# Kernel tuning notes

Hardware: AMD Instinct MI355X
Metric: run time of the kernel (lower is better)

## Reference

```python
import jax, jax.numpy as jnp
import numpy as np

NEG_SLOPE = 0.2
EPS = 1e-16


def _gat_layer(x, src, dst, W, a_src, a_dst, b, n_nodes):
    # x: [N, Fin], W: [Fout, Fin]; src/dst: [E'] (self-loops already appended)
    h = x @ W.T                              # [N, Fout]
    alpha_s = h @ a_src                      # [N] per-source score
    alpha_d = h @ a_dst                      # [N] per-dest score
    e = jax.nn.leaky_relu(alpha_s[src] + alpha_d[dst], NEG_SLOPE)  # [E']
    # segment softmax over destination nodes (PyG softmax semantics)
    m = jax.ops.segment_max(e, dst, num_segments=n_nodes)          # [N]
    ex = jnp.exp(e - m[dst])                                       # [E']
    s = jax.ops.segment_sum(ex, dst, num_segments=n_nodes)         # [N]
    alpha = ex / (s[dst] + EPS)                                    # [E']
    out = jax.ops.segment_sum(alpha[:, None] * h[src], dst, num_segments=n_nodes)
    return out + b, alpha


def setup_inputs() -> dict:
    key = jax.random.key(0)
    ks = jax.random.split(key, 14)
    N, E, F_IN, H1, H2, F_OUT = 50000, 800000, 128, 64, 64, 32
    sc = 0.1
    return {
        "x": jax.random.normal(ks[0], (N, F_IN), dtype=jnp.float32),
        "edge_index": jax.random.randint(ks[1], (2, E), 0, N, dtype=jnp.int64),
        "W1": jax.random.normal(ks[2], (H1, F_IN), dtype=jnp.float32) * sc,
        "a_src1": jax.random.normal(ks[3], (H1,), dtype=jnp.float32) * sc,
        "a_dst1": jax.random.normal(ks[4], (H1,), dtype=jnp.float32) * sc,
        "b1": jnp.zeros((H1,), dtype=jnp.float32),
        "W2": jax.random.normal(ks[5], (H2, H1), dtype=jnp.float32) * sc,
        "a_src2": jax.random.normal(ks[6], (H2,), dtype=jnp.float32) * sc,
        "a_dst2": jax.random.normal(ks[7], (H2,), dtype=jnp.float32) * sc,
        "b2": jnp.zeros((H2,), dtype=jnp.float32),
        "W3": jax.random.normal(ks[8], (F_OUT, H2), dtype=jnp.float32) * sc,
        "a_src3": jax.random.normal(ks[9], (F_OUT,), dtype=jnp.float32) * sc,
        "a_dst3": jax.random.normal(ks[10], (F_OUT,), dtype=jnp.float32) * sc,
        "b3": jnp.zeros((F_OUT,), dtype=jnp.float32),
    }


def reference(x, edge_index, W1, a_src1, a_dst1, b1, W2, a_src2, a_dst2, b2, W3, a_src3, a_dst3, b3):
    N = x.shape[0]
    loops = jnp.arange(N, dtype=edge_index.dtype)
    src = jnp.concatenate([edge_index[0], loops])  # add_self_loops=True
    dst = jnp.concatenate([edge_index[1], loops])

    h, alpha1 = _gat_layer(x, src, dst, W1, a_src1, a_dst1, b1, N)
    h = jax.nn.relu(h)
    h, _ = _gat_layer(h, src, dst, W2, a_src2, a_dst2, b2, N)
    h = jax.nn.relu(h)
    out, _ = _gat_layer(h, src, dst, W3, a_src3, a_dst3, b3, N)
    # att_tuple = (edge_index with self loops, attention coefficients of layer 1)
    return (jnp.stack([src, dst]), alpha1, out)
```

## Files before the change

kernel.cpp:

```cpp
#include <hip/hip_runtime.h>
#include <hip/hip_bf16.h>
#include <math.h>

#define NEG_SLOPE 0.2f
#define GAT_EPS 1e-16f

constexpr int NN = 50000;
constexpr int NE = 800000;
constexpr int EP = NE + NN;
constexpr int NB = (NN + 255) / 256;

constexpr int PB  = 128;
constexpr int PT  = 1024;
constexpr int CH  = (EP + PB - 1) / PB;
constexpr int NCH = 4;
constexpr int BPC = PB / NCH;

__device__ inline void edge_sd(const int* __restrict__ ei, int i, int& s, int& d) {
    if (i < NE) { s = ei[i]; d = ei[NE + i]; }
    else        { s = d = i - NE; }
}

__device__ inline float bflo(unsigned int h) { return __uint_as_float(h << 16); }
__device__ inline float bfhi(unsigned int h) { return __uint_as_float(h & 0xffff0000u); }

__global__ __launch_bounds__(PT) void k_p1_hist(const int* __restrict__ ei,
                                                float* __restrict__ out0,
                                                unsigned char* __restrict__ hist,
                                                unsigned char* __restrict__ rank8) {
    __shared__ unsigned int sh[NN / 4];
    int b = blockIdx.x, t = threadIdx.x;
    for (int w = t; w < NN / 4; w += PT) sh[w] = 0u;
    __syncthreads();
    int i0 = b * CH;
    int iend = i0 + CH; if (iend > EP) iend = EP;
    for (int i = i0 + t; i < iend; i += PT) {
        int s, d; edge_sd(ei, i, s, d);
        __builtin_nontemporal_store((float)s, &out0[i]);
        __builtin_nontemporal_store((float)d, &out0[EP + i]);
        int sft = (d & 3) * 8;
        unsigned int old = atomicAdd(&sh[d >> 2], 1u << sft);
        __builtin_nontemporal_store((unsigned char)(old >> sft), &rank8[i]);
    }
    __syncthreads();
    unsigned int* hw = (unsigned int*)(hist + (size_t)b * NN);
    for (int w = t; w < NN / 4; w += PT) hw[w] = sh[w];
}

__global__ __launch_bounds__(256) void k_p2s1(unsigned char* __restrict__ hist,
                                              unsigned char* __restrict__ chunkoff,
                                              int* __restrict__ rowptr,
                                              int* __restrict__ bsum) {
    __shared__ int sh[256];
    int t = threadIdx.x;
    int n = blockIdx.x * 256 + t;
    int v = 0;
    if (n < NN) {
        unsigned int runs[NCH];
#pragma unroll
        for (int c = 0; c < NCH; ++c) {
            size_t base = (size_t)(c * BPC) * NN + n;
            unsigned int vv[BPC];
#pragma unroll
            for (int b = 0; b < BPC; ++b) vv[b] = hist[base + (size_t)b * NN];
            unsigned int run = 0;
#pragma unroll
            for (int b = 0; b < BPC; ++b) { unsigned int x = vv[b]; vv[b] = run; run += x; }
#pragma unroll
            for (int b = 0; b < BPC; ++b) hist[base + (size_t)b * NN] = (unsigned char)vv[b];
            runs[c] = run;
        }
        unsigned int o1 = runs[0], o2 = o1 + runs[1], o3 = o2 + runs[2];
        *(unsigned int*)&chunkoff[(size_t)n * 4] = (o1 << 8) | (o2 << 16) | (o3 << 24);
        v = (int)(o3 + runs[3]);
    }
    sh[t] = v; __syncthreads();
    for (int off = 1; off < 256; off <<= 1) {
        int x = (t >= off) ? sh[t - off] : 0;
        __syncthreads();
        sh[t] += x;
        __syncthreads();
    }
    if (n < NN) rowptr[n] = sh[t] - v;
    if (t == 255) bsum[blockIdx.x] = sh[255];
}

__global__ __launch_bounds__(256) void k_s23(int* __restrict__ rowptr,
                                             const int* __restrict__ bsum) {
    __shared__ int sh[256];
    int t = threadIdx.x;
    int v = (t < NB) ? bsum[t] : 0;
    sh[t] = v; __syncthreads();
    for (int off = 1; off < 256; off <<= 1) {
        int x = (t >= off) ? sh[t - off] : 0;
        __syncthreads();
        sh[t] += x;
        __syncthreads();
    }
    int blk = blockIdx.x;
    int off = (blk == 0) ? 0 : sh[blk - 1];
    int n = blk * 256 + t;
    if (n < NN) rowptr[n] += off;
    if (n == 0) rowptr[NN] = EP;
}

__global__ __launch_bounds__(256) void k_fill(const int* __restrict__ ei,
                                              const unsigned char* __restrict__ rank8,
                                              const unsigned char* __restrict__ hist,
                                              const unsigned char* __restrict__ chunkoff,
                                              const int* __restrict__ rowptr,
                                              unsigned short* __restrict__ col) {
    int i = blockIdx.x * 256 + threadIdx.x;
    if (i >= EP) return;
    int b = i / CH;
    int c = b / BPC;
    int s, d; edge_sd(ei, i, s, d);
    int pos = rowptr[d] + (int)chunkoff[d * 4 + c] + (int)hist[(size_t)b * NN + d]
            + (int)rank8[i];
    col[pos] = (unsigned short)s;
}

__global__ void k_alpha_out(const int* __restrict__ ei, const float* __restrict__ as_,
                            const float* __restrict__ ad_, const float* __restrict__ inv,
                            float* __restrict__ out_alpha) {
    int i = blockIdx.x * blockDim.x + threadIdx.x;
    if (i >= EP) return;
    int s, d; edge_sd(ei, i, s, d);
    float v = as_[s] + ad_[d];
    v = v > 0.f ? v : NEG_SLOPE * v;
    __builtin_nontemporal_store(__expf(v) * inv[d], &out_alpha[i]);
}

struct alignas(8) bh4 { __hip_bfloat16 a, b, c, d; };

__device__ inline void fma4(float4& acc, float x, const float4& w) {
    acc.x = fmaf(x, w.x, acc.x);
    acc.y = fmaf(x, w.y, acc.y);
    acc.z = fmaf(x, w.z, acc.z);
    acc.w = fmaf(x, w.w, acc.w);
}

template <int FIN, int FOUT, int NPB>
__global__ __launch_bounds__(256) void k_gemm_t(const float* __restrict__ in,
                                                const float* __restrict__ W,
                                                const float* __restrict__ avs,
                                                const float* __restrict__ avd,
                                                __hip_bfloat16* __restrict__ H,
                                                float* __restrict__ as_,
                                                float* __restrict__ ad_, int n) {
    constexpr int TF = FOUT / 4;
    constexpr int XS = FIN + 4;
    constexpr int WS = FOUT + 4;
    __shared__ float sX[NPB * XS];
    __shared__ float sWt[FIN * WS];
    int tid = threadIdx.x;
    for (int idx = tid; idx < FIN * FOUT; idx += 256) {
        int f = idx % FOUT, k = idx / FOUT;
        sWt[k * WS + f] = W[f * FIN + k];
    }
    int nb = blockIdx.x * NPB;
    for (int idx = tid; idx < NPB * (FIN / 4); idx += 256) {
        int node = idx / (FIN / 4), kq = idx % (FIN / 4);
        int g = nb + node;
        float4 v = make_float4(0.f, 0.f, 0.f, 0.f);
        if (g < n) v = *(const float4*)&in[(size_t)g * FIN + kq * 4];
        *(float4*)&sX[node * XS + kq * 4] = v;
    }
    __syncthreads();

    int fq = tid % TF, ng = tid / TF;
    int n0 = ng * 4;
    float4 acc0 = make_float4(0.f, 0.f, 0.f, 0.f);
    float4 acc1 = acc0, acc2 = acc0, acc3 = acc0;
    for (int k = 0; k < FIN; k += 4) {
        float4 w0 = *(const float4*)&sWt[(k + 0) * WS + fq * 4];
        float4 w1 = *(const float4*)&sWt[(k + 1) * WS + fq * 4];
        float4 w2 = *(const float4*)&sWt[(k + 2) * WS + fq * 4];
        float4 w3 = *(const float4*)&sWt[(k + 3) * WS + fq * 4];
        float4 x0 = *(const float4*)&sX[(n0 + 0) * XS + k];
        float4 x1 = *(const float4*)&sX[(n0 + 1) * XS + k];
        float4 x2 = *(const float4*)&sX[(n0 + 2) * XS + k];
        float4 x3 = *(const float4*)&sX[(n0 + 3) * XS + k];
        fma4(acc0, x0.x, w0); fma4(acc0, x0.y, w1); fma4(acc0, x0.z, w2); fma4(acc0, x0.w, w3);
        fma4(acc1, x1.x, w0); fma4(acc1, x1.y, w1); fma4(acc1, x1.z, w2); fma4(acc1, x1.w, w3);
        fma4(acc2, x2.x, w0); fma4(acc2, x2.y, w1); fma4(acc2, x2.z, w2); fma4(acc2, x2.w, w3);
        fma4(acc3, x3.x, w0); fma4(acc3, x3.y, w1); fma4(acc3, x3.z, w2); fma4(acc3, x3.w, w3);
    }
    float4 accs[4] = {acc0, acc1, acc2, acc3};
    float4 vs4 = *(const float4*)&avs[fq * 4];
    float4 vd4 = *(const float4*)&avd[fq * 4];
#pragma unroll
    for (int j = 0; j < 4; ++j) {
        int g = nb + n0 + j;
        float ps = accs[j].x * vs4.x + accs[j].y * vs4.y + accs[j].z * vs4.z + accs[j].w * vs4.w;
        float pd = accs[j].x * vd4.x + accs[j].y * vd4.y + accs[j].z * vd4.z + accs[j].w * vd4.w;
#pragma unroll
        for (int off = TF / 2; off; off >>= 1) {
            ps += __shfl_down(ps, off, TF);
            pd += __shfl_down(pd, off, TF);
        }
        if (g < n) {
            if (fq == 0) { as_[g] = ps; ad_[g] = pd; }
            bh4 o;
            o.a = __float2bfloat16(accs[j].x);
            o.b = __float2bfloat16(accs[j].y);
            o.c = __float2bfloat16(accs[j].z);
            o.d = __float2bfloat16(accs[j].w);
            *(bh4*)&H[(size_t)g * FOUT + fq * 4] = o;
        }
    }
}

template <int FOUT, bool RELU, bool WRITE_INV>
__global__ __launch_bounds__(256) void k_node_attn(
    const int* __restrict__ rowptr, const unsigned short* __restrict__ col,
    const float* __restrict__ as_, const float* __restrict__ ad_,
    const __hip_bfloat16* __restrict__ H, const float* __restrict__ bias,
    float* __restrict__ outp, float* __restrict__ inv_out) {
    int wid = (blockIdx.x * blockDim.x + threadIdx.x) >> 6;
    int lane = threadIdx.x & 63;
    if (wid >= NN) return;
    int start = rowptr[wid], end = rowptr[wid + 1];
    float adv = ad_[wid];
    const uint2* __restrict__ H4 = (const uint2*)H;

    float sloc = 0.f;
    float ax = 0.f, ay = 0.f, az = 0.f, aw = 0.f;
    for (int c = start; c < end; c += 64) {
        int e = c + lane;
        float p = 0.f;
        int sc = 0;
        if (e < end) {
            sc = (int)col[e];
            float v = as_[sc] + adv;
            v = v > 0.f ? v : NEG_SLOPE * v;
            p = __expf(v);
        }
        sloc += p;
        int cnt = end - c; if (cnt > 64) cnt = 64;
        if (FOUT == 64) {
            int q = lane >> 4, fl = lane & 15;
            int j = 0;
            for (; j + 32 <= cnt; j += 32) {
                float pp[8]; int ss[8]; uint2 hh[8];
#pragma unroll
                for (int k = 0; k < 8; ++k) {
                    int ek = j + 4 * k + q;
                    pp[k] = __shfl(p, ek);
                    ss[k] = __shfl(sc, ek);
                }
#pragma unroll
                for (int k = 0; k < 8; ++k) hh[k] = H4[((size_t)ss[k] << 4) + fl];
#pragma unroll
                for (int k = 0; k < 8; ++k) {
                    ax = fmaf(pp[k], bflo(hh[k].x), ax);
                    ay = fmaf(pp[k], bfhi(hh[k].x), ay);
                    az = fmaf(pp[k], bflo(hh[k].y), az);
                    aw = fmaf(pp[k], bfhi(hh[k].y), aw);
                }
            }
            for (; j + 8 <= cnt; j += 8) {
                int e0 = j + q, e1 = j + 4 + q;
                float p0 = __shfl(p, e0), p1 = __shfl(p, e1);
                int s0 = __shfl(sc, e0), s1 = __shfl(sc, e1);
                uint2 h0 = H4[((size_t)s0 << 4) + fl];
                uint2 h1 = H4[((size_t)s1 << 4) + fl];
                ax = fmaf(p0, bflo(h0.x), ax); ay = fmaf(p0, bfhi(h0.x), ay);
                az = fmaf(p0, bflo(h0.y), az); aw = fmaf(p0, bfhi(h0.y), aw);
                ax = fmaf(p1, bflo(h1.x), ax); ay = fmaf(p1, bfhi(h1.x), ay);
                az = fmaf(p1, bflo(h1.y), az); aw = fmaf(p1, bfhi(h1.y), aw);
            }
            for (; j < cnt; j += 4) {
                int e0 = j + q;
                float p0 = __shfl(p, e0);
                int   s0 = __shfl(sc, e0);
                uint2 h0 = H4[((size_t)s0 << 4) + fl];
                ax = fmaf(p0, bflo(h0.x), ax); ay = fmaf(p0, bfhi(h0.x), ay);
                az = fmaf(p0, bflo(h0.y), az); aw = fmaf(p0, bfhi(h0.y), aw);
            }
        } else {
            int oc = lane >> 3, fl = lane & 7;
            int j = 0;
            for (; j + 32 <= cnt; j += 32) {
                float pp[4]; int ss[4]; uint2 hh[4];
#pragma unroll
                for (int k = 0; k < 4; ++k) {
                    int ek = j + 8 * k + oc;
                    pp[k] = __shfl(p, ek);
                    ss[k] = __shfl(sc, ek);
                }
#pragma unroll
                for (int k = 0; k < 4; ++k) hh[k] = H4[((size_t)ss[k] << 3) + fl];
#pragma unroll
                for (int k = 0; k < 4; ++k) {
                    ax = fmaf(pp[k], bflo(hh[k].x), ax);
                    ay = fmaf(pp[k], bfhi(hh[k].x), ay);
                    az = fmaf(pp[k], bflo(hh[k].y), az);
                    aw = fmaf(pp[k], bfhi(hh[k].y), aw);
                }
            }
            for (; j < cnt; j += 8) {
                int e0 = j + oc;
                float p0 = __shfl(p, e0);
                int   s0 = __shfl(sc, e0);
                uint2 h0 = H4[((size_t)s0 << 3) + fl];
                ax = fmaf(p0, bflo(h0.x), ax); ay = fmaf(p0, bfhi(h0.x), ay);
                az = fmaf(p0, bflo(h0.y), az); aw = fmaf(p0, bfhi(h0.y), aw);
            }
        }
    }
    for (int off = 32; off; off >>= 1) sloc += __shfl_xor(sloc, off);
    float inv = 1.f / (sloc + GAT_EPS);
    if (WRITE_INV && lane == 0) inv_out[wid] = inv;

    if (FOUT == 64) {
        ax += __shfl_xor(ax, 16); ay += __shfl_xor(ay, 16);
        az += __shfl_xor(az, 16); aw += __shfl_xor(aw, 16);
        ax += __shfl_xor(ax, 32); ay += __shfl_xor(ay, 32);
        az += __shfl_xor(az, 32); aw += __shfl_xor(aw, 32);
        if (lane < 16) {
            float4 bb = *(const float4*)&bias[lane * 4];
            float o0 = bb.x + ax * inv;
            float o1 = bb.y + ay * inv;
            float o2 = bb.z + az * inv;
            float o3 = bb.w + aw * inv;
            if (RELU) {
                o0 = fmaxf(o0, 0.f); o1 = fmaxf(o1, 0.f);
                o2 = fmaxf(o2, 0.f); o3 = fmaxf(o3, 0.f);
            }
            *(float4*)&outp[((size_t)wid << 6) + lane * 4] = make_float4(o0, o1, o2, o3);
        }
    } else {
        ax += __shfl_xor(ax, 8);  ay += __shfl_xor(ay, 8);
        az += __shfl_xor(az, 8);  aw += __shfl_xor(aw, 8);
        ax += __shfl_xor(ax, 16); ay += __shfl_xor(ay, 16);
        az += __shfl_xor(az, 16); aw += __shfl_xor(aw, 16);
        ax += __shfl_xor(ax, 32); ay += __shfl_xor(ay, 32);
        az += __shfl_xor(az, 32); aw += __shfl_xor(aw, 32);
        if (lane < 8) {
            float4 bb = *(const float4*)&bias[lane * 4];
            float o0 = bb.x + ax * inv;
            float o1 = bb.y + ay * inv;
            float o2 = bb.z + az * inv;
            float o3 = bb.w + aw * inv;
            if (RELU) {
                o0 = fmaxf(o0, 0.f); o1 = fmaxf(o1, 0.f);
                o2 = fmaxf(o2, 0.f); o3 = fmaxf(o3, 0.f);
            }
            *(float4*)&outp[((size_t)wid << 5) + lane * 4] = make_float4(o0, o1, o2, o3);
        }
    }
}

extern "C" void kernel_launch(void* const* d_in, const int* in_sizes, int n_in,
                              void* d_out, int out_size, void* d_ws, size_t ws_size,
                              hipStream_t stream) {
    const float* x  = (const float*)d_in[0];
    const int*   ei = (const int*)d_in[1];
    const float* W1 = (const float*)d_in[2];
    const float* as1 = (const float*)d_in[3];
    const float* ad1 = (const float*)d_in[4];
    const float* b1 = (const float*)d_in[5];
    const float* W2 = (const float*)d_in[6];
    const float* as2 = (const float*)d_in[7];
    const float* ad2 = (const float*)d_in[8];
    const float* b2 = (const float*)d_in[9];
    const float* W3 = (const float*)d_in[10];
    const float* as3 = (const float*)d_in[11];
    const float* ad3 = (const float*)d_in[12];
    const float* b3 = (const float*)d_in[13];

    float* out = (float*)d_out;
    float* out_edges = out;
    float* out_alpha = out + 2 * EP;
    float* out_final = out + 3 * EP;

    char* w = (char*)d_ws;
    size_t o = 0;
    auto alloc = [&](size_t bytes) { void* p = w + o; o = (o + bytes + 15) & ~15ull; return p; };
    float* as_ = (float*)alloc((size_t)NN * 4);
    float* ad_ = (float*)alloc((size_t)NN * 4);
    float* inv = (float*)alloc((size_t)NN * 4);
    __hip_bfloat16* H = (__hip_bfloat16*)alloc((size_t)NN * 64 * 2);
    int* rowptr = (int*)alloc((size_t)(NN + 1) * 4);
    unsigned char* rank8 = (unsigned char*)alloc((size_t)EP);
    unsigned short* col  = (unsigned short*)alloc((size_t)EP * 2);
    unsigned char* chunkoff = (unsigned char*)alloc((size_t)NN * 4);
    int* bsum = (int*)alloc(1024);

    const size_t aggBytes  = (size_t)NN * 64 * 4;
    const size_t histBytes = (size_t)PB * NN;
    float* agg = (ws_size >= o + aggBytes)
        ? (float*)(w + o)
        : (float*)d_in[0];
    unsigned char* hist = (ws_size >= o + aggBytes + histBytes)
        ? (unsigned char*)(w + o + aggBytes)
        : (unsigned char*)out_final;

    k_p1_hist<<<PB, PT, 0, stream>>>(ei, out_edges, hist, rank8);
    k_p2s1<<<NB, 256, 0, stream>>>(hist, chunkoff, rowptr, bsum);
    k_s23<<<NB, 256, 0, stream>>>(rowptr, bsum);
    k_fill<<<(EP + 255) / 256, 256, 0, stream>>>(ei, rank8, hist, chunkoff, rowptr, col);

    const int nblk = (NN * 64 + 255) / 256;

    k_gemm_t<128, 64, 64><<<(NN + 63) / 64, 256, 0, stream>>>(x, W1, as1, ad1, H, as_, ad_, NN);
    k_node_attn<64, true, true><<<nblk, 256, 0, stream>>>(rowptr, col, as_, ad_, H, b1,
                                                          agg, inv);
    k_alpha_out<<<(EP + 255) / 256, 256, 0, stream>>>(ei, as_, ad_, inv, out_alpha);

    k_gemm_t<64, 64, 64><<<(NN + 63) / 64, 256, 0, stream>>>(agg, W2, as2, ad2, H, as_, ad_, NN);
    k_node_attn<64, true, false><<<nblk, 256, 0, stream>>>(rowptr, col, as_, ad_, H, b2,
                                                           agg, nullptr);

    k_gemm_t<64, 32, 128><<<(NN + 127) / 128, 256, 0, stream>>>(agg, W3, as3, ad3, H, as_, ad_,
                                                                NN);
    k_node_attn<32, false, false><<<nblk, 256, 0, stream>>>(rowptr, col, as_, ad_, H, b3,
                                                            out_final, nullptr);
}
```

Before: 292.7 us.

## Fuse attention aggregation with next layer's linear transform and scores

Adds a kernel that aggregates attention-weighted neighbor features per destination node, applies bias and ReLU, then multiplies by the next layer's weight matrix held in shared memory and computes the next layer's source/destination scores. This removes two separate GEMM launches and the fp32 intermediate round trip through global memory. Separate H/score buffers per layer avoid read-write hazards. It also drops the 8-edge unrolled tail in the old aggregation kernel. The risk is that each block now stages the weights in shared memory and each wave does extra shuffle work, which could lower occupancy.

```diff
diff --git a/kernel.cpp b/kernel.cpp
--- a/kernel.cpp
+++ b/kernel.cpp
@@ -211,6 +211,150 @@
     }
 }
 
+template <int GOUT, bool WRITE_INV>
+__global__ __launch_bounds__(256) void k_attn_gemm(
+    const int* __restrict__ rowptr, const unsigned short* __restrict__ col,
+    const float* __restrict__ as_, const float* __restrict__ ad_,
+    const __hip_bfloat16* __restrict__ H, const float* __restrict__ bias,
+    const float* __restrict__ Wn,
+    const float* __restrict__ avs, const float* __restrict__ avd,
+    __hip_bfloat16* __restrict__ Hout,
+    float* __restrict__ as_out, float* __restrict__ ad_out,
+    float* __restrict__ inv_out) {
+    __shared__ float sW[64 * GOUT];
+    int tid = threadIdx.x;
+    for (int idx = tid; idx < 64 * GOUT; idx += 256) {
+        int f = idx % GOUT, k = idx / GOUT;
+        sW[k * GOUT + f] = Wn[f * 64 + k];
+    }
+    __syncthreads();
+
+    int wid = (blockIdx.x * blockDim.x + tid) >> 6;
+    int lane = tid & 63;
+    if (wid >= NN) return;
+    int start = rowptr[wid], end = rowptr[wid + 1];
+    float adv = ad_[wid];
+    const uint2* __restrict__ H4 = (const uint2*)H;
+
+    float sloc = 0.f;
+    float ax = 0.f, ay = 0.f, az = 0.f, aw = 0.f;
+    for (int c = start; c < end; c += 64) {
+        int e = c + lane;
+        float p = 0.f;
+        int sc = 0;
+        if (e < end) {
+            sc = (int)col[e];
+            float v = as_[sc] + adv;
+            v = v > 0.f ? v : NEG_SLOPE * v;
+            p = __expf(v);
+        }
+        sloc += p;
+        int cnt = end - c; if (cnt > 64) cnt = 64;
+        int q = lane >> 4, fl = lane & 15;
+        int j = 0;
+        for (; j + 32 <= cnt; j += 32) {
+            float pp[8]; int ss[8]; uint2 hh[8];
+#pragma unroll
+            for (int k = 0; k < 8; ++k) {
+                int ek = j + 4 * k + q;
+                pp[k] = __shfl(p, ek);
+                ss[k] = __shfl(sc, ek);
+            }
+#pragma unroll
+            for (int k = 0; k < 8; ++k) hh[k] = H4[((size_t)ss[k] << 4) + fl];
+#pragma unroll
+            for (int k = 0; k < 8; ++k) {
+                ax = fmaf(pp[k], bflo(hh[k].x), ax);
+                ay = fmaf(pp[k], bfhi(hh[k].x), ay);
+                az = fmaf(pp[k], bflo(hh[k].y), az);
+                aw = fmaf(pp[k], bfhi(hh[k].y), aw);
+            }
+        }
+        for (; j + 8 <= cnt; j += 8) {
+            int e0 = j + q, e1 = j + 4 + q;
+            float p0 = __shfl(p, e0), p1 = __shfl(p, e1);
+            int s0 = __shfl(sc, e0), s1 = __shfl(sc, e1);
+            uint2 h0 = H4[((size_t)s0 << 4) + fl];
+            uint2 h1 = H4[((size_t)s1 << 4) + fl];
+            ax = fmaf(p0, bflo(h0.x), ax); ay = fmaf(p0, bfhi(h0.x), ay);
+            az = fmaf(p0, bflo(h0.y), az); aw = fmaf(p0, bfhi(h0.y), aw);
+            ax = fmaf(p1, bflo(h1.x), ax); ay = fmaf(p1, bfhi(h1.x), ay);
+            az = fmaf(p1, bflo(h1.y), az); aw = fmaf(p1, bfhi(h1.y), aw);
+        }
+        for (; j < cnt; j += 4) {
+            int e0 = j + q;
+            float p0 = __shfl(p, e0);
+            int   s0 = __shfl(sc, e0);
+            uint2 h0 = H4[((size_t)s0 << 4) + fl];
+            ax = fmaf(p0, bflo(h0.x), ax); ay = fmaf(p0, bfhi(h0.x), ay);
+            az = fmaf(p0, bflo(h0.y), az); aw = fmaf(p0, bfhi(h0.y), aw);
+        }
+    }
+    for (int off = 32; off; off >>= 1) sloc += __shfl_xor(sloc, off);
+    float inv = 1.f / (sloc + GAT_EPS);
+    if (WRITE_INV && lane == 0) inv_out[wid] = inv;
+
+    ax += __shfl_xor(ax, 16); ay += __shfl_xor(ay, 16);
+    az += __shfl_xor(az, 16); aw += __shfl_xor(aw, 16);
+    ax += __shfl_xor(ax, 32); ay += __shfl_xor(ay, 32);
+    az += __shfl_xor(az, 32); aw += __shfl_xor(aw, 32);
+
+    int fl = lane & 15;
+    float4 bb = *(const float4*)&bias[fl * 4];
+    float h0 = fmaxf(bb.x + ax * inv, 0.f);
+    float h1 = fmaxf(bb.y + ay * inv, 0.f);
+    float h2 = fmaxf(bb.z + az * inv, 0.f);
+    float h3 = fmaxf(bb.w + aw * inv, 0.f);
+
+    float acc = 0.f;
+    if (GOUT == 64) {
+        int f = lane;
+#pragma unroll
+        for (int m = 0; m < 16; ++m) {
+            float q0 = __shfl(h0, m), q1 = __shfl(h1, m);
+            float q2 = __shfl(h2, m), q3 = __shfl(h3, m);
+            acc = fmaf(q0, sW[(4 * m + 0) * 64 + f], acc);
+            acc = fmaf(q1, sW[(4 * m + 1) * 64 + f], acc);
+            acc = fmaf(q2, sW[(4 * m + 2) * 64 + f], acc);
+            acc = fmaf(q3, sW[(4 * m + 3) * 64 + f], acc);
+        }
+    } else {
+        int f = lane & 31, kh = lane >> 5;
+#pragma unroll
+        for (int mm = 0; mm < 8; ++mm) {
+            int m = 8 * kh + mm;
+            float q0 = __shfl(h0, m), q1 = __shfl(h1, m);
+            float q2 = __shfl(h2, m), q3 = __shfl(h3, m);
+            acc = fmaf(q0, sW[(4 * m + 0) * 32 + f], acc);
+            acc = fmaf(q1, sW[(4 * m + 1) * 32 + f], acc);
+            acc = fmaf(q2, sW[(4 * m + 2) * 32 + f], acc);
+            acc = fmaf(q3, sW[(4 * m + 3) * 32 + f], acc);
+        }
+        acc += __shfl_xor(acc, 32);
+    }
+
+    float ps, pd;
+    if (GOUT == 64) {
+        ps = acc * avs[lane];
+        pd = acc * avd[lane];
+    } else {
+        ps = (lane < 32) ? acc * avs[lane] : 0.f;
+        pd = (lane < 32) ? acc * avd[lane] : 0.f;
+    }
+#pragma unroll
+    for (int off = 32; off; off >>= 1) {
+        ps += __shfl_xor(ps, off);
+        pd += __shfl_xor(pd, off);
+    }
+    if (lane == 0) { as_out[wid] = ps; ad_out[wid] = pd; }
+
+    if (GOUT == 64) {
+        Hout[(size_t)wid * 64 + lane] = __float2bfloat16(acc);
+    } else if (lane < 32) {
+        Hout[(size_t)wid * 32 + lane] = __float2bfloat16(acc);
+    }
+}
+
 template <int FOUT, bool RELU, bool WRITE_INV>
 __global__ __launch_bounds__(256) void k_node_attn(
     const int* __restrict__ rowptr, const unsigned short* __restrict__ col,
@@ -258,17 +402,6 @@
                     az = fmaf(pp[k], bflo(hh[k].y), az);
                     aw = fmaf(pp[k], bfhi(hh[k].y), aw);
                 }
-            }
-            for (; j + 8 <= cnt; j += 8) {
-                int e0 = j + q, e1 = j + 4 + q;
-                float p0 = __shfl(p, e0), p1 = __shfl(p, e1);
-                int s0 = __shfl(sc, e0), s1 = __shfl(sc, e1);
-                uint2 h0 = H4[((size_t)s0 << 4) + fl];
-                uint2 h1 = H4[((size_t)s1 << 4) + fl];
-                ax = fmaf(p0, bflo(h0.x), ax); ay = fmaf(p0, bfhi(h0.x), ay);
-                az = fmaf(p0, bflo(h0.y), az); aw = fmaf(p0, bfhi(h0.y), aw);
-                ax = fmaf(p1, bflo(h1.x), ax); ay = fmaf(p1, bfhi(h1.x), ay);
-                az = fmaf(p1, bflo(h1.y), az); aw = fmaf(p1, bfhi(h1.y), aw);
             }
             for (; j < cnt; j += 4) {
                 int e0 = j + q;
@@ -378,23 +511,25 @@
     char* w = (char*)d_ws;
     size_t o = 0;
     auto alloc = [&](size_t bytes) { void* p = w + o; o = (o + bytes + 15) & ~15ull; return p; };
-    float* as_ = (float*)alloc((size_t)NN * 4);
-    float* ad_ = (float*)alloc((size_t)NN * 4);
+    float* asA = (float*)alloc((size_t)NN * 4);
+    float* adA = (float*)alloc((size_t)NN * 4);
+    float* asB = (float*)alloc((size_t)NN * 4);
+    float* adB = (float*)alloc((size_t)NN * 4);
+    float* asC = (float*)alloc((size_t)NN * 4);
+    float* adC = (float*)alloc((size_t)NN * 4);
     float* inv = (float*)alloc((size_t)NN * 4);
-    __hip_bfloat16* H = (__hip_bfloat16*)alloc((size_t)NN * 64 * 2);
+    __hip_bfloat16* H1 = (__hip_bfloat16*)alloc((size_t)NN * 64 * 2);
+    __hip_bfloat16* H2 = (__hip_bfloat16*)alloc((size_t)NN * 64 * 2);
+    __hip_bfloat16* H3 = (__hip_bfloat16*)alloc((size_t)NN * 32 * 2);
     int* rowptr = (int*)alloc((size_t)(NN + 1) * 4);
     unsigned char* rank8 = (unsigned char*)alloc((size_t)EP);
     unsigned short* col  = (unsigned short*)alloc((size_t)EP * 2);
     unsigned char* chunkoff = (unsigned char*)alloc((size_t)NN * 4);
     int* bsum = (int*)alloc(1024);
 
-    const size_t aggBytes  = (size_t)NN * 64 * 4;
     const size_t histBytes = (size_t)PB * NN;
-    float* agg = (ws_size >= o + aggBytes)
-        ? (float*)(w + o)
-        : (float*)d_in[0];
-    unsigned char* hist = (ws_size >= o + aggBytes + histBytes)
-        ? (unsigned char*)(w + o + aggBytes)
+    unsigned char* hist = (ws_size >= o + histBytes)
+        ? (unsigned char*)(w + o)
         : (unsigned char*)out_final;
 
     k_p1_hist<<<PB, PT, 0, stream>>>(ei, out_edges, hist, rank8);
@@ -404,17 +539,14 @@
 
     const int nblk = (NN * 64 + 255) / 256;
 
-    k_gemm_t<128, 64, 64><<<(NN + 63) / 64, 256, 0, stream>>>(x, W1, as1, ad1, H, as_, ad_, NN);
-    k_node_attn<64, true, true><<<nblk, 256, 0, stream>>>(rowptr, col, as_, ad_, H, b1,
-                                                          agg, inv);
-    k_alpha_out<<<(EP + 255) / 256, 256, 0, stream>>>(ei, as_, ad_, inv, out_alpha);
-
-    k_gemm_t<64, 64, 64><<<(NN + 63) / 64, 256, 0, stream>>>(agg, W2, as2, ad2, H, as_, ad_, NN);
-    k_node_attn<64, true, false><<<nblk, 256, 0, stream>>>(rowptr, col, as_, ad_, H, b2,
-                                                           agg, nullptr);
-
-    k_gemm_t<64, 32, 128><<<(NN + 127) / 128, 256, 0, stream>>>(agg, W3, as3, ad3, H, as_, ad_,
-                                                                NN);
-    k_node_attn<32, false, false><<<nblk, 256, 0, stream>>>(rowptr, col, as_, ad_, H, b3,
+    k_gemm_t<128, 64, 64><<<(NN + 63) / 64, 256, 0, stream>>>(x, W1, as1, ad1, H1,
+                                                              asA, adA, NN);
+    k_attn_gemm<64, true><<<nblk, 256, 0, stream>>>(rowptr, col, asA, adA, H1, b1,
+                                                    W2, as2, ad2, H2, asB, adB, inv);
+    k_alpha_out<<<(EP + 255) / 256, 256, 0, stream>>>(ei, asA, adA, inv, out_alpha);
+
+    k_attn_gemm<32, false><<<nblk, 256, 0, stream>>>(rowptr, col, asB, adB, H2, b2,
+                                                     W3, as3, ad3, H3, asC, adC, nullptr);
+    k_node_attn<32, false, false><<<nblk, 256, 0, stream>>>(rowptr, col, asC, adC, H3, b3,
                                                             out_final, nullptr);
 }
```

After: 390.1 us. 33.3% more time.

## Map multiple destination nodes per wavefront in attention aggregation

Applied to the files above, without the earlier changes.

The attention aggregation kernel now assigns a 16-lane (FOUT=64) or 8-lane (FOUT=32) group to each destination node instead of a full 64-lane wavefront, so one wave handles 4 or 8 nodes at once. Average degree is about 17, so a full wave per node left most lanes idle in the score phase and needed wide cross-lane reductions. Edges are processed 8 at a time per group, and per-group shuffles broadcast scores and source indices. The cost is fewer independent gathers in flight per node and load imbalance between nodes of different degree in the same wave.

```diff
diff --git a/kernel.cpp b/kernel.cpp
--- a/kernel.cpp
+++ b/kernel.cpp
@@ -212,144 +212,74 @@
 }
 
 template <int FOUT, bool RELU, bool WRITE_INV>
-__global__ __launch_bounds__(256) void k_node_attn(
+__global__ __launch_bounds__(256) void k_attn_grp(
     const int* __restrict__ rowptr, const unsigned short* __restrict__ col,
     const float* __restrict__ as_, const float* __restrict__ ad_,
     const __hip_bfloat16* __restrict__ H, const float* __restrict__ bias,
     float* __restrict__ outp, float* __restrict__ inv_out) {
-    int wid = (blockIdx.x * blockDim.x + threadIdx.x) >> 6;
+    constexpr int L = (FOUT == 64) ? 16 : 8;
+    constexpr int GPW = 64 / L;
+    int tid = blockIdx.x * 256 + threadIdx.x;
+    int wid = tid >> 6;
     int lane = threadIdx.x & 63;
-    if (wid >= NN) return;
-    int start = rowptr[wid], end = rowptr[wid + 1];
-    float adv = ad_[wid];
+    int grp = lane / L;
+    int gl  = lane & (L - 1);
+    int node = wid * GPW + grp;
+    if (node >= NN) return;
+
+    int start = rowptr[node], end = rowptr[node + 1];
+    float adv = ad_[node];
     const uint2* __restrict__ H4 = (const uint2*)H;
+    int base = lane & ~(L - 1);
 
     float sloc = 0.f;
-    float ax = 0.f, ay = 0.f, az = 0.f, aw = 0.f;
-    for (int c = start; c < end; c += 64) {
-        int e = c + lane;
+    float4 acc = make_float4(0.f, 0.f, 0.f, 0.f);
+    for (int c = start; c < end; c += 8) {
+        int e = c + gl;
         float p = 0.f;
         int sc = 0;
-        if (e < end) {
+        if (gl < 8 && e < end) {
             sc = (int)col[e];
             float v = as_[sc] + adv;
             v = v > 0.f ? v : NEG_SLOPE * v;
             p = __expf(v);
         }
         sloc += p;
-        int cnt = end - c; if (cnt > 64) cnt = 64;
-        if (FOUT == 64) {
-            int q = lane >> 4, fl = lane & 15;
-            int j = 0;
-            for (; j + 32 <= cnt; j += 32) {
-                float pp[8]; int ss[8]; uint2 hh[8];
-#pragma unroll
-                for (int k = 0; k < 8; ++k) {
-                    int ek = j + 4 * k + q;
-                    pp[k] = __shfl(p, ek);
-                    ss[k] = __shfl(sc, ek);
-                }
-#pragma unroll
-                for (int k = 0; k < 8; ++k) hh[k] = H4[((size_t)ss[k] << 4) + fl];
-#pragma unroll
-                for (int k = 0; k < 8; ++k) {
-                    ax = fmaf(pp[k], bflo(hh[k].x), ax);
-                    ay = fmaf(pp[k], bfhi(hh[k].x), ay);
-                    az = fmaf(pp[k], bflo(hh[k].y), az);
-                    aw = fmaf(pp[k], bfhi(hh[k].y), aw);
-                }
-            }
-            for (; j + 8 <= cnt; j += 8) {
-                int e0 = j + q, e1 = j + 4 + q;
-                float p0 = __shfl(p, e0), p1 = __shfl(p, e1);
-                int s0 = __shfl(sc, e0), s1 = __shfl(sc, e1);
-                uint2 h0 = H4[((size_t)s0 << 4) + fl];
-                uint2 h1 = H4[((size_t)s1 << 4) + fl];
-                ax = fmaf(p0, bflo(h0.x), ax); ay = fmaf(p0, bfhi(h0.x), ay);
-                az = fmaf(p0, bflo(h0.y), az); aw = fmaf(p0, bfhi(h0.y), aw);
-                ax = fmaf(p1, bflo(h1.x), ax); ay = fmaf(p1, bfhi(h1.x), ay);
-                az = fmaf(p1, bflo(h1.y), az); aw = fmaf(p1, bfhi(h1.y), aw);
-            }
-            for (; j < cnt; j += 4) {
-                int e0 = j + q;
-                float p0 = __shfl(p, e0);
-                int   s0 = __shfl(sc, e0);
-                uint2 h0 = H4[((size_t)s0 << 4) + fl];
-                ax = fmaf(p0, bflo(h0.x), ax); ay = fmaf(p0, bfhi(h0.x), ay);
-                az = fmaf(p0, bflo(h0.y), az); aw = fmaf(p0, bfhi(h0.y), aw);
-            }
-        } else {
-            int oc = lane >> 3, fl = lane & 7;
-            int j = 0;
-            for (; j + 32 <= cnt; j += 32) {
-                float pp[4]; int ss[4]; uint2 hh[4];
-#pragma unroll
-                for (int k = 0; k < 4; ++k) {
-                    int ek = j + 8 * k + oc;
-                    pp[k] = __shfl(p, ek);
-                    ss[k] = __shfl(sc, ek);
-                }
-#pragma unroll
-                for (int k = 0; k < 4; ++k) hh[k] = H4[((size_t)ss[k] << 3) + fl];
-#pragma unroll
-                for (int k = 0; k < 4; ++k) {
-                    ax = fmaf(pp[k], bflo(hh[k].x), ax);
-                    ay = fmaf(pp[k], bfhi(hh[k].x), ay);
-                    az = fmaf(pp[k], bflo(hh[k].y), az);
-                    aw = fmaf(pp[k], bfhi(hh[k].y), aw);
-                }
-            }
-            for (; j < cnt; j += 8) {
-                int e0 = j + oc;
-                float p0 = __shfl(p, e0);
-                int   s0 = __shfl(sc, e0);
-                uint2 h0 = H4[((size_t)s0 << 3) + fl];
-                ax = fmaf(p0, bflo(h0.x), ax); ay = fmaf(p0, bfhi(h0.x), ay);
-                az = fmaf(p0, bflo(h0.y), az); aw = fmaf(p0, bfhi(h0.y), aw);
-            }
-        }
-    }
-    for (int off = 32; off; off >>= 1) sloc += __shfl_xor(sloc, off);
+        int cnt = end - c; if (cnt > 8) cnt = 8;
+        float pp[8]; int ss[8]; uint2 hh[8];
+#pragma unroll
+        for (int k = 0; k < 8; ++k) {
+            pp[k] = __shfl(p, base + k);
+            ss[k] = __shfl(sc, base + k);
+        }
+#pragma unroll
+        for (int k = 0; k < 8; ++k) {
+            hh[k] = make_uint2(0u, 0u);
+            if (k < cnt) hh[k] = H4[(size_t)ss[k] * L + gl];
+        }
+#pragma unroll
+        for (int k = 0; k < 8; ++k) {
+            acc.x = fmaf(pp[k], bflo(hh[k].x), acc.x);
+            acc.y = fmaf(pp[k], bfhi(hh[k].x), acc.y);
+            acc.z = fmaf(pp[k], bflo(hh[k].y), acc.z);
+            acc.w = fmaf(pp[k], bfhi(hh[k].y), acc.w);
+        }
+    }
+#pragma unroll
+    for (int off = L / 2; off; off >>= 1) sloc += __shfl_xor(sloc, off);
     float inv = 1.f / (sloc + GAT_EPS);
-    if (WRITE_INV && lane == 0) inv_out[wid] = inv;
-
-    if (FOUT == 64) {
-        ax += __shfl_xor(ax, 16); ay += __shfl_xor(ay, 16);
-        az += __shfl_xor(az, 16); aw += __shfl_xor(aw, 16);
-        ax += __shfl_xor(ax, 32); ay += __shfl_xor(ay, 32);
-        az += __shfl_xor(az, 32); aw += __shfl_xor(aw, 32);
-        if (lane < 16) {
-            float4 bb = *(const float4*)&bias[lane * 4];
-            float o0 = bb.x + ax * inv;
-            float o1 = bb.y + ay * inv;
-            float o2 = bb.z + az * inv;
-            float o3 = bb.w + aw * inv;
-            if (RELU) {
-                o0 = fmaxf(o0, 0.f); o1 = fmaxf(o1, 0.f);
-                o2 = fmaxf(o2, 0.f); o3 = fmaxf(o3, 0.f);
-            }
-            *(float4*)&outp[((size_t)wid << 6) + lane * 4] = make_float4(o0, o1, o2, o3);
-        }
-    } else {
-        ax += __shfl_xor(ax, 8);  ay += __shfl_xor(ay, 8);
-        az += __shfl_xor(az, 8);  aw += __shfl_xor(aw, 8);
-        ax += __shfl_xor(ax, 16); ay += __shfl_xor(ay, 16);
-        az += __shfl_xor(az, 16); aw += __shfl_xor(aw, 16);
-        ax += __shfl_xor(ax, 32); ay += __shfl_xor(ay, 32);
-        az += __shfl_xor(az, 32); aw += __shfl_xor(aw, 32);
-        if (lane < 8) {
-            float4 bb = *(const float4*)&bias[lane * 4];
-            float o0 = bb.x + ax * inv;
-            float o1 = bb.y + ay * inv;
-            float o2 = bb.z + az * inv;
-            float o3 = bb.w + aw * inv;
-            if (RELU) {
-                o0 = fmaxf(o0, 0.f); o1 = fmaxf(o1, 0.f);
-                o2 = fmaxf(o2, 0.f); o3 = fmaxf(o3, 0.f);
-            }
-            *(float4*)&outp[((size_t)wid << 5) + lane * 4] = make_float4(o0, o1, o2, o3);
-        }
-    }
+    if (WRITE_INV && gl == 0) inv_out[node] = inv;
+
+    float4 bb = *(const float4*)&bias[gl * 4];
+    float o0 = bb.x + acc.x * inv;
+    float o1 = bb.y + acc.y * inv;
+    float o2 = bb.z + acc.z * inv;
+    float o3 = bb.w + acc.w * inv;
+    if (RELU) {
+        o0 = fmaxf(o0, 0.f); o1 = fmaxf(o1, 0.f);
+        o2 = fmaxf(o2, 0.f); o3 = fmaxf(o3, 0.f);
+    }
+    *(float4*)&outp[(size_t)node * FOUT + gl * 4] = make_float4(o0, o1, o2, o3);
 }
 
 extern "C" void kernel_launch(void* const* d_in, const int* in_sizes, int n_in,
@@ -402,19 +332,20 @@
     k_s23<<<NB, 256, 0, stream>>>(rowptr, bsum);
     k_fill<<<(EP + 255) / 256, 256, 0, stream>>>(ei, rank8, hist, chunkoff, rowptr, col);
 
-    const int nblk = (NN * 64 + 255) / 256;
+    const int nblk64 = (NN + 15) / 16;
+    const int nblk32 = (NN + 31) / 32;
 
     k_gemm_t<128, 64, 64><<<(NN + 63) / 64, 256, 0, stream>>>(x, W1, as1, ad1, H, as_, ad_, NN);
-    k_node_attn<64, true, true><<<nblk, 256, 0, stream>>>(rowptr, col, as_, ad_, H, b1,
-                                                          agg, inv);
+    k_attn_grp<64, true, true><<<nblk64, 256, 0, stream>>>(rowptr, col, as_, ad_, H, b1,
+                                                           agg, inv);
     k_alpha_out<<<(EP + 255) / 256, 256, 0, stream>>>(ei, as_, ad_, inv, out_alpha);
 
     k_gemm_t<64, 64, 64><<<(NN + 63) / 64, 256, 0, stream>>>(agg, W2, as2, ad2, H, as_, ad_, NN);
-    k_node_attn<64, true, false><<<nblk, 256, 0, stream>>>(rowptr, col, as_, ad_, H, b2,
-                                                           agg, nullptr);
+    k_attn_grp<64, true, false><<<nblk64, 256, 0, stream>>>(rowptr, col, as_, ad_, H, b2,
+                                                            agg, nullptr);
 
     k_gemm_t<64, 32, 128><<<(NN + 127) / 128, 256, 0, stream>>>(agg, W3, as3, ad3, H, as_, ad_,
                                                                 NN);
-    k_node_attn<32, false, false><<<nblk, 256, 0, stream>>>(rowptr, col, as_, ad_, H, b3,
-                                                            out_final, nullptr);
-}
+    k_attn_grp<32, false, false><<<nblk32, 256, 0, stream>>>(rowptr, col, as_, ad_, H, b3,
+                                                             out_final, nullptr);
+}
```

Result: faster. 273.1 us, median of 2 (-6.7%).
